# Kernel tuning notes

Hardware: AMD Instinct MI355X
Metric: run time of the kernel (lower is better)

The kernel has to match this reference:

```python
import jax, jax.numpy as jnp
import numpy as np

N_NODES = 50000
N_EDGES = 800000
EPS = 1e-16

def _gat_layer(x, row, col, W, a_src, a_dst, b, heads, concat):
    N = x.shape[0]
    C = a_src.shape[1]
    h = (x @ W).reshape(N, heads, C)                       # [N,H,C]
    al_src = jnp.sum(h * a_src, axis=-1)                    # [N,H]
    al_dst = jnp.sum(h * a_dst, axis=-1)                    # [N,H]
    e = jax.nn.leaky_relu(al_src[row] + al_dst[col], 0.2)   # [E,H]
    # segment softmax over destination node (col)
    m = jax.ops.segment_max(e, col, num_segments=N)
    e = jnp.exp(e - m[col])
    s = jax.ops.segment_sum(e, col, num_segments=N)
    alpha = e / (s[col] + EPS)                              # [E,H]
    msg = h[row] * alpha[:, :, None]                        # [E,H,C]
    out = jax.ops.segment_sum(msg, col, num_segments=N)     # [N,H,C]
    out = out.reshape(N, heads * C) if concat else out.mean(axis=1)
    return out + b

def setup_inputs() -> dict:
    key = jax.random.key(0)
    ks = jax.random.split(key, 16)
    d_in, hid, d_out, d_edge, H = 64, 64, 32, 16, 4
    inp = {
        "x": jax.random.normal(ks[0], (N_NODES, d_in), jnp.float32),
        "edge_index": jax.random.randint(ks[1], (2, N_EDGES), 0, N_NODES, jnp.int32),
        "edge_attr": jax.random.normal(ks[2], (N_EDGES, d_edge), jnp.float32),
        "W1": jax.random.normal(ks[3], (d_in, H * hid), jnp.float32) * 0.1,
        "a1_src": jax.random.normal(ks[4], (H, hid), jnp.float32) * 0.1,
        "a1_dst": jax.random.normal(ks[5], (H, hid), jnp.float32) * 0.1,
        "b1": jax.random.normal(ks[6], (H * hid,), jnp.float32) * 0.1,
        "W2": jax.random.normal(ks[7], (H * hid, hid), jnp.float32) * 0.05,
        "a2_src": jax.random.normal(ks[8], (1, hid), jnp.float32) * 0.1,
        "a2_dst": jax.random.normal(ks[9], (1, hid), jnp.float32) * 0.1,
        "b2": jax.random.normal(ks[10], (hid,), jnp.float32) * 0.1,
        "Wn": jax.random.normal(ks[11], (hid, d_out), jnp.float32) * 0.1,
        "bn": jax.random.normal(ks[12], (d_out,), jnp.float32) * 0.1,
        "We": jax.random.normal(ks[13], (2 * hid + d_edge, 1), jnp.float32) * 0.1,
        "be": jax.random.normal(ks[14], (1,), jnp.float32) * 0.1,
    }
    return inp

def reference(x, edge_index, edge_attr, W1, a1_src, a1_dst, b1, W2, a2_src, a2_dst, b2, Wn, bn, We, be):
    N = x.shape[0]
    row0, col0 = edge_index[0], edge_index[1]
    # PyG GATConv default: add self loops for message passing
    loops = jnp.arange(N, dtype=edge_index.dtype)
    row = jnp.concatenate([row0, loops])
    col = jnp.concatenate([col0, loops])
    h = jax.nn.elu(_gat_layer(x, row, col, W1, a1_src, a1_dst, b1, heads=4, concat=True))
    h = jax.nn.elu(_gat_layer(h, row, col, W2, a2_src, a2_dst, b2, heads=1, concat=False))
    node_out = h @ Wn + bn                                   # [N, out]
    edge_feat = jnp.concatenate([h[row0], h[col0], edge_attr], axis=1)  # [E, 2*hid+d_edge]
    edge_out = edge_feat @ We + be                           # [E, 1]
    return (node_out, edge_out)
```

## Files before the change

kernel.cpp:

```cpp
#include <hip/hip_runtime.h>
#include <hip/hip_bf16.h>

#define N_NODES 50000
#define N_EDGES 800000
#define N_TOT   850000
#define MAXD    128

#define NBUCK 196
#define BCAP  8192

typedef __hip_bfloat16 bf16;
typedef __attribute__((ext_vector_type(8))) short bf16x8;
typedef __attribute__((ext_vector_type(4))) float f32x4;

__device__ __forceinline__ unsigned short f2bu(float v){
  union { bf16 b; unsigned short u; } cv; cv.b = __float2bfloat16(v); return cv.u;
}
__device__ __forceinline__ float bflo(unsigned int d){ return __uint_as_float(d << 16); }
__device__ __forceinline__ float bfhi(unsigned int d){ return __uint_as_float(d & 0xffff0000u); }

__global__ __launch_bounds__(256) void wfrag_kernel(const float* __restrict__ W1, const float* __restrict__ W2,
    const float* __restrict__ a1s, const float* __restrict__ a1d,
    unsigned short* __restrict__ wf1, unsigned short* __restrict__ wf2,
    float* __restrict__ ws1, float* __restrict__ wd1, int* __restrict__ bcur){
  int b = blockIdx.x, tid = threadIdx.x;
  if (b < 128) {
    int i = b*256 + tid;
    if (i < 16384) {
      int k = i >> 8, n = i & 255;
      int kk = k >> 5, qq = (k >> 3) & 3, j = k & 7, nt = n >> 4, cc = n & 15;
      wf1[(((kk*16 + nt)*4 + qq)*16 + cc)*8 + j] = f2bu(W1[i]);
    } else {
      int i2 = i - 16384;
      int k = i2 >> 6, n = i2 & 63;
      int kk = k >> 5, qq = (k >> 3) & 3, j = k & 7, ch = n >> 4, cc = n & 15;
      wf2[(((kk*4 + ch)*4 + qq)*16 + cc)*8 + j] = f2bu(W2[i2]);
    }
  } else if (b == 128) {
    int k = tid >> 2, h = tid & 3;
    const float* wrow = W1 + k*256 + h*64;
    const float* as = a1s + h*64;
    const float* ad = a1d + h*64;
    float ss = 0.f, sd = 0.f;
    #pragma unroll 8
    for (int c = 0; c < 64; ++c) {
      float wv = wrow[c];
      ss = fmaf(wv, as[c], ss);
      sd = fmaf(wv, ad[c], sd);
    }
    ws1[k*4 + h] = ss;
    wd1[k*4 + h] = sd;
  } else {
    if (tid < NBUCK) bcur[tid] = 0;
  }
}

__global__ __launch_bounds__(256) void binscatter_kernel(const int* __restrict__ ei,
    int* __restrict__ bcur, unsigned int* __restrict__ pairbuf){
  __shared__ int hist[NBUCK];
  __shared__ int gbase[NBUCK];
  int tid = threadIdx.x;
  if (tid < NBUCK) hist[tid] = 0;
  __syncthreads();
  int base = blockIdx.x * 4096;
  #pragma unroll 4
  for (int i = 0; i < 16; ++i) {
    int k = base + i*256 + tid;
    if (k < N_TOT) {
      int c = (k < N_EDGES) ? ei[N_EDGES + k] : (k - N_EDGES);
      atomicAdd(&hist[c >> 8], 1);
    }
  }
  __syncthreads();
  if (tid < NBUCK) {
    int h = hist[tid];
    gbase[tid] = h ? (tid*BCAP + atomicAdd(&bcur[tid], h)) : 0;
    hist[tid] = 0;
  }
  __syncthreads();
  #pragma unroll 4
  for (int i = 0; i < 16; ++i) {
    int k = base + i*256 + tid;
    if (k < N_TOT) {
      int r, c;
      if (k < N_EDGES) { r = ei[k]; c = ei[N_EDGES + k]; } else { r = c = k - N_EDGES; }
      int b = c >> 8;
      int lpos = atomicAdd(&hist[b], 1);
      pairbuf[gbase[b] + lpos] = (unsigned)r | ((unsigned)(c & 255) << 16);
    }
  }
}

__global__ __launch_bounds__(256) void lscatter2_kernel(const unsigned int* __restrict__ pairbuf,
    const int* __restrict__ bcur, int* __restrict__ offs, int* __restrict__ srcs){
  __shared__ int sbase[256];
  __shared__ int lhist[256];
  __shared__ int lcur[256];
  int b = blockIdx.x, tid = threadIdx.x;
  int sz = 0;
  if (tid < NBUCK) {
    sz = bcur[tid];
    if (sz < 0) sz = 0; if (sz > BCAP) sz = BCAP;
  }
  sbase[tid] = sz;
  lhist[tid] = 0;
  __syncthreads();
  for (int off = 1; off < 256; off <<= 1) {
    int t = (tid >= off) ? sbase[tid - off] : 0;
    __syncthreads();
    sbase[tid] += t;
    __syncthreads();
  }
  int bbase_b = (b == 0) ? 0 : sbase[b - 1];
  int size = sbase[b] - bbase_b;
  int base = b * BCAP;
  for (int j = tid; j < size; j += 256)
    atomicAdd(&lhist[pairbuf[base + j] >> 16], 1);
  __syncthreads();
  int v = lhist[tid];
  lcur[tid] = v;
  __syncthreads();
  for (int off = 1; off < 256; off <<= 1) {
    int t = (tid >= off) ? lcur[tid - off] : 0;
    __syncthreads();
    lcur[tid] += t;
    __syncthreads();
  }
  int excl = lcur[tid] - v;
  int gpos = bbase_b + excl;
  int node = b*256 + tid;
  if (node < N_NODES) offs[node] = gpos;
  if (b == 0 && tid == 0) offs[N_NODES] = N_TOT;
  __syncthreads();
  lcur[tid] = gpos;
  __syncthreads();
  for (int j = tid; j < size; j += 256) {
    unsigned pv = pairbuf[base + j];
    int pos = atomicAdd(&lcur[pv >> 16], 1);
    srcs[pos] = (int)(pv & 0xFFFFu);
  }
}

__global__ __launch_bounds__(256) void xprep_kernel(const float* __restrict__ x,
    const float* __restrict__ ws1, const float* __restrict__ wd1,
    unsigned short* __restrict__ xb, float* __restrict__ al1s, float* __restrict__ al1d){
  __shared__ float sws[64][4], swd[64][4];
  int tid = threadIdx.x;
  sws[tid >> 2][tid & 3] = ws1[tid];
  swd[tid >> 2][tid & 3] = wd1[tid];
  __syncthreads();
  int lane = tid & 63, wave = tid >> 6;
  int g = lane & 15, sub = lane >> 4;
  int n = blockIdx.x*16 + wave*4 + sub;
  float4 xv = *(const float4*)(x + (size_t)n*64 + g*4);
  uint2 dd;
  dd.x = (unsigned)f2bu(xv.x) | ((unsigned)f2bu(xv.y) << 16);
  dd.y = (unsigned)f2bu(xv.z) | ((unsigned)f2bu(xv.w) << 16);
  ((uint2*)xb)[(size_t)n*16 + g] = dd;
  int c0 = g*4;
  float ps0 = 0.f, ps1 = 0.f, ps2 = 0.f, ps3 = 0.f;
  float pd0 = 0.f, pd1 = 0.f, pd2 = 0.f, pd3 = 0.f;
  float xc[4] = {xv.x, xv.y, xv.z, xv.w};
  #pragma unroll
  for (int i = 0; i < 4; ++i) {
    int c = c0 + i;
    ps0 = fmaf(xc[i], sws[c][0], ps0); ps1 = fmaf(xc[i], sws[c][1], ps1);
    ps2 = fmaf(xc[i], sws[c][2], ps2); ps3 = fmaf(xc[i], sws[c][3], ps3);
    pd0 = fmaf(xc[i], swd[c][0], pd0); pd1 = fmaf(xc[i], swd[c][1], pd1);
    pd2 = fmaf(xc[i], swd[c][2], pd2); pd3 = fmaf(xc[i], swd[c][3], pd3);
  }
  #pragma unroll
  for (int off = 1; off < 16; off <<= 1) {
    ps0 += __shfl_xor(ps0, off, 64); ps1 += __shfl_xor(ps1, off, 64);
    ps2 += __shfl_xor(ps2, off, 64); ps3 += __shfl_xor(ps3, off, 64);
    pd0 += __shfl_xor(pd0, off, 64); pd1 += __shfl_xor(pd1, off, 64);
    pd2 += __shfl_xor(pd2, off, 64); pd3 += __shfl_xor(pd3, off, 64);
  }
  if (g < 4)      al1s[(size_t)n*4 + g]       = (g==0)?ps0:(g==1)?ps1:(g==2)?ps2:ps3;
  else if (g < 8) al1d[(size_t)n*4 + (g-4)]   = (g==4)?pd0:(g==5)?pd1:(g==6)?pd2:pd3;
}

__global__ __launch_bounds__(256, 8) void attn1x_kernel(const unsigned short* __restrict__ xb,
    const float* __restrict__ al1s, const float* __restrict__ al1d,
    const int* __restrict__ offs, const int* __restrict__ srcs,
    bf16* __restrict__ ag){
  __shared__ __align__(16) float ebuf[4][MAXD+4][4];
  __shared__ int sbuf[4][MAXD+4];

  int wave = threadIdx.x >> 6, lane = threadIdx.x & 63;
  int n = blockIdx.x*4 + wave;
  int start = offs[n], end = offs[n+1];
  int deg = end - start;
  int lim = deg < MAXD ? deg : MAXD;
  float4 aldv = *(const float4*)(al1d + (size_t)n*4);
  float ald0 = aldv.x, ald1 = aldv.y, ald2 = aldv.z, ald3 = aldv.w;

  float s0 = 0.f, s1 = 0.f, s2 = 0.f, s3 = 0.f;
  {
    int idx = lane;
    for (int j = start + lane; j < end; j += 64, idx += 64) {
      int r = srcs[j];
      float4 als = *(const float4*)(al1s + (size_t)r*4);
      float e0 = als.x + ald0; e0 = e0 >= 0.f ? e0 : 0.2f*e0; float p0 = __expf(e0); s0 += p0;
      float e1 = als.y + ald1; e1 = e1 >= 0.f ? e1 : 0.2f*e1; float p1 = __expf(e1); s1 += p1;
      float e2 = als.z + ald2; e2 = e2 >= 0.f ? e2 : 0.2f*e2; float p2 = __expf(e2); s2 += p2;
      float e3 = als.w + ald3; e3 = e3 >= 0.f ? e3 : 0.2f*e3; float p3 = __expf(e3); s3 += p3;
      if (idx < MAXD) {
        sbuf[wave][idx] = r;
        *(float4*)&ebuf[wave][idx][0] = make_float4(p0, p1, p2, p3);
      }
    }
  }
  if (lane < 4) {
    int ip = lim + lane;
    sbuf[wave][ip] = 0;
    *(float4*)&ebuf[wave][ip][0] = make_float4(0.f, 0.f, 0.f, 0.f);
  }
  #pragma unroll
  for (int off = 32; off; off >>= 1) {
    s0 += __shfl_xor(s0, off, 64);
    s1 += __shfl_xor(s1, off, 64);
    s2 += __shfl_xor(s2, off, 64);
    s3 += __shfl_xor(s3, off, 64);
  }
  float inv0 = 1.f/(s0 + 1e-16f), inv1 = 1.f/(s1 + 1e-16f);
  float inv2 = 1.f/(s2 + 1e-16f), inv3 = 1.f/(s3 + 1e-16f);

  int cl = lane & 15, es = lane >> 4;
  float acc[4][4];
  #pragma unroll
  for (int h = 0; h < 4; ++h)
    #pragma unroll
    for (int i = 0; i < 4; ++i) acc[h][i] = 0.f;
  {
    const uint2* base2 = (const uint2*)xb;
    #pragma unroll 2
    for (int jj = 0; jj < lim; jj += 4) {
      int idx = jj + es;
      int r = sbuf[wave][idx];
      float4 pv = *(const float4*)&ebuf[wave][idx][0];
      uint2 d = base2[(size_t)r*16 + cl];
      float c0 = bflo(d.x), c1 = bfhi(d.x), c2 = bflo(d.y), c3 = bfhi(d.y);
      acc[0][0] = fmaf(pv.x, c0, acc[0][0]); acc[0][1] = fmaf(pv.x, c1, acc[0][1]);
      acc[0][2] = fmaf(pv.x, c2, acc[0][2]); acc[0][3] = fmaf(pv.x, c3, acc[0][3]);
      acc[1][0] = fmaf(pv.y, c0, acc[1][0]); acc[1][1] = fmaf(pv.y, c1, acc[1][1]);
      acc[1][2] = fmaf(pv.y, c2, acc[1][2]); acc[1][3] = fmaf(pv.y, c3, acc[1][3]);
      acc[2][0] = fmaf(pv.z, c0, acc[2][0]); acc[2][1] = fmaf(pv.z, c1, acc[2][1]);
      acc[2][2] = fmaf(pv.z, c2, acc[2][2]); acc[2][3] = fmaf(pv.z, c3, acc[2][3]);
      acc[3][0] = fmaf(pv.w, c0, acc[3][0]); acc[3][1] = fmaf(pv.w, c1, acc[3][1]);
      acc[3][2] = fmaf(pv.w, c2, acc[3][2]); acc[3][3] = fmaf(pv.w, c3, acc[3][3]);
    }
  }
  if (deg > MAXD) {
    const uint2* base2 = (const uint2*)xb;
    for (int jj = MAXD; jj < deg; jj += 4) {
      int idx = jj + es;
      bool ok = idx < deg;
      int j = ok ? (start + idx) : start;
      int r = srcs[j];
      float4 als = *(const float4*)(al1s + (size_t)r*4);
      float e0 = als.x + ald0; e0 = e0 >= 0.f ? e0 : 0.2f*e0; float p0 = __expf(e0);
      float e1 = als.y + ald1; e1 = e1 >= 0.f ? e1 : 0.2f*e1; float p1 = __expf(e1);
      float e2 = als.z + ald2; e2 = e2 >= 0.f ? e2 : 0.2f*e2; float p2 = __expf(e2);
      float e3 = als.w + ald3; e3 = e3 >= 0.f ? e3 : 0.2f*e3; float p3 = __expf(e3);
      float m = ok ? 1.f : 0.f;
      uint2 d = base2[(size_t)r*16 + cl];
      float c0 = bflo(d.x)*m, c1 = bfhi(d.x)*m, c2 = bflo(d.y)*m, c3 = bfhi(d.y)*m;
      acc[0][0] = fmaf(p0, c0, acc[0][0]); acc[0][1] = fmaf(p0, c1, acc[0][1]);
      acc[0][2] = fmaf(p0, c2, acc[0][2]); acc[0][3] = fmaf(p0, c3, acc[0][3]);
      acc[1][0] = fmaf(p1, c0, acc[1][0]); acc[1][1] = fmaf(p1, c1, acc[1][1]);
      acc[1][2] = fmaf(p1, c2, acc[1][2]); acc[1][3] = fmaf(p1, c3, acc[1][3]);
      acc[2][0] = fmaf(p2, c0, acc[2][0]); acc[2][1] = fmaf(p2, c1, acc[2][1]);
      acc[2][2] = fmaf(p2, c2, acc[2][2]); acc[2][3] = fmaf(p2, c3, acc[2][3]);
      acc[3][0] = fmaf(p3, c0, acc[3][0]); acc[3][1] = fmaf(p3, c1, acc[3][1]);
      acc[3][2] = fmaf(p3, c2, acc[3][2]); acc[3][3] = fmaf(p3, c3, acc[3][3]);
    }
  }
  #pragma unroll
  for (int h = 0; h < 4; ++h)
    #pragma unroll
    for (int i = 0; i < 4; ++i) {
      acc[h][i] += __shfl_xor(acc[h][i], 16, 64);
      acc[h][i] += __shfl_xor(acc[h][i], 32, 64);
    }
  {
    float invh = (es==0)?inv0:(es==1)?inv1:(es==2)?inv2:inv3;
    float o0 = ((es==0)?acc[0][0]:(es==1)?acc[1][0]:(es==2)?acc[2][0]:acc[3][0]) * invh;
    float o1 = ((es==0)?acc[0][1]:(es==1)?acc[1][1]:(es==2)?acc[2][1]:acc[3][1]) * invh;
    float o2 = ((es==0)?acc[0][2]:(es==1)?acc[1][2]:(es==2)?acc[2][2]:acc[3][2]) * invh;
    float o3 = ((es==0)?acc[0][3]:(es==1)?acc[1][3]:(es==2)?acc[2][3]:acc[3][3]) * invh;
    uint2 dd;
    dd.x = (unsigned)f2bu(o0) | ((unsigned)f2bu(o1) << 16);
    dd.y = (unsigned)f2bu(o2) | ((unsigned)f2bu(o3) << 16);
    ((uint2*)ag)[(size_t)n*64 + lane] = dd;
  }
}

__global__ __launch_bounds__(256) void gemm1b_kernel(const unsigned short* __restrict__ ag,
    const unsigned short* __restrict__ wf1, const float* __restrict__ b1, bf16* __restrict__ h1){
  __shared__ __align__(16) unsigned short ctile[32*264];
  int tid = threadIdx.x, wave = tid >> 6, lane = tid & 63;
  int q = lane >> 4, c = lane & 15;
  int n0 = blockIdx.x * 64;

  union { uint4 u; bf16x8 v; } bfr[2][4];
  #pragma unroll
  for (int kk = 0; kk < 2; ++kk)
    #pragma unroll
    for (int nti = 0; nti < 4; ++nti)
      bfr[kk][nti].u = *(const uint4*)(wf1 + (size_t)((((kk*16 + wave*4 + nti)*4 + q)*16 + c)*8));

  float b1v[4];
  #pragma unroll
  for (int nti = 0; nti < 4; ++nti) b1v[nti] = b1[(wave*4 + nti)*16 + c];

  #pragma unroll
  for (int half = 0; half < 2; ++half) {
    #pragma unroll
    for (int sti = 0; sti < 2; ++sti) {
      int st = half*2 + sti;
      int row = n0 + st*16 + c;
      if (row >= N_NODES) row = N_NODES - 1;
      bf16x8 afr[2];
      #pragma unroll
      for (int kk = 0; kk < 2; ++kk) {
        union { uint4 u; bf16x8 v; } a;
        a.u = *(const uint4*)(ag + (size_t)row*256 + wave*64 + kk*32 + q*8);
        afr[kk] = a.v;
      }
      #pragma unroll
      for (int nti = 0; nti < 4; ++nti) {
        f32x4 acc = {0.f, 0.f, 0.f, 0.f};
        #pragma unroll
        for (int kk = 0; kk < 2; ++kk)
          acc = __builtin_amdgcn_mfma_f32_16x16x32_bf16(afr[kk], bfr[kk][nti].v, acc, 0, 0, 0);
        int lrow = sti*16 + q*4, nt = wave*4 + nti;
        #pragma unroll
        for (int r = 0; r < 4; ++r) {
          float o = acc[r] + b1v[nti];
          o = o > 0.f ? o : expm1f(o);
          ctile[(lrow + r)*264 + nt*16 + c] = f2bu(o);
        }
      }
    }
    __syncthreads();
    #pragma unroll 1
    for (int i = 0; i < 8; ++i) {
      int lr = wave*8 + i;
      int node = n0 + half*32 + lr;
      if (node < N_NODES) {
        uint2 dd = *(const uint2*)&ctile[lr*264 + lane*4];
        ((uint2*)h1)[(size_t)node*64 + lane] = dd;
      }
    }
    __syncthreads();
  }
}

__global__ __launch_bounds__(256) void gemm2_kernel(const bf16* __restrict__ h1, const unsigned short* __restrict__ wf2,
    const float* __restrict__ a2s, const float* __restrict__ a2d,
    bf16* __restrict__ h2pre, float* __restrict__ al2s, float* __restrict__ al2d){
  __shared__ __align__(16) float ctile[64][65];
  int tid = threadIdx.x, wave = tid >> 6, lane = tid & 63;
  int q = lane >> 4, c = lane & 15;
  int n0 = blockIdx.x * 64;

  union { uint4 u; bf16x8 v; } bfr[8];
  #pragma unroll
  for (int kk = 0; kk < 8; ++kk)
    bfr[kk].u = *(const uint4*)(wf2 + (size_t)((((kk*4 + wave)*4 + q)*16 + c)*8));

  const unsigned short* h1u = (const unsigned short*)h1;
  #pragma unroll 1
  for (int st = 0; st < 4; ++st) {
    if (n0 + st*16 >= N_NODES) break;
    f32x4 acc = {0.f, 0.f, 0.f, 0.f};
    size_t arow = (size_t)(n0 + st*16 + c)*256 + q*8;
    #pragma unroll
    for (int kk = 0; kk < 8; ++kk) {
      union { uint4 u; bf16x8 v; } a;
      a.u = *(const uint4*)(h1u + arow + kk*32);
      acc = __builtin_amdgcn_mfma_f32_16x16x32_bf16(a.v, bfr[kk].v, acc, 0, 0, 0);
    }
    #pragma unroll
    for (int r = 0; r < 4; ++r)
      ctile[st*16 + q*4 + r][wave*16 + c] = acc[r];
  }
  __syncthreads();

  float as = a2s[lane], ad = a2d[lane];
  #pragma unroll 1
  for (int i = 0; i < 16; ++i) {
    int node = n0 + wave*16 + i;
    if (node >= N_NODES) break;
    float val = ctile[wave*16 + i][lane];
    ((unsigned short*)h2pre)[(size_t)node*64 + lane] = f2bu(val);
    float ps = val*as, pd = val*ad;
    #pragma unroll
    for (int off = 32; off; off >>= 1) { ps += __shfl_xor(ps, off, 64); pd += __shfl_xor(pd, off, 64); }
    if (lane == 0) { al2s[node] = ps; al2d[node] = pd; }
  }
}

__global__ __launch_bounds__(512, 8) void attn2_kernel(const bf16* __restrict__ h2pre,
    const float* __restrict__ al2s, const float* __restrict__ al2d,
    const int* __restrict__ offs, const int* __restrict__ srcs,
    const float* __restrict__ b2, float* __restrict__ h2f){
  __shared__ float ebuf[8][MAXD+8];
  __shared__ int   sbuf[8][MAXD+8];
  int wave = threadIdx.x >> 6, lane = threadIdx.x & 63;
  int n = blockIdx.x*8 + wave;
  int start = offs[n], end = offs[n+1];
  int deg = end - start;
  int lim = deg < MAXD ? deg : MAXD;
  float ald = al2d[n];

  float sm = 0.f;
  {
    int idx = lane;
    for (int j = start + lane; j < end; j += 64, idx += 64) {
      int r = srcs[j];
      float t = al2s[r] + ald; t = t >= 0.f ? t : 0.2f*t;
      float p = __expf(t); sm += p;
      if (idx < MAXD) { sbuf[wave][idx] = r; ebuf[wave][idx] = p; }
    }
  }
  if (lane < 8) { int ip = lim + lane; sbuf[wave][ip] = 0; ebuf[wave][ip] = 0.f; }
  #pragma unroll
  for (int off = 32; off; off >>= 1) sm += __shfl_xor(sm, off, 64);
  float inv = 1.f/(sm + 1e-16f);

  int cl = lane & 7, es = lane >> 3;
  float acc0 = 0.f, acc1 = 0.f, acc2 = 0.f, acc3 = 0.f;
  float acc4 = 0.f, acc5 = 0.f, acc6 = 0.f, acc7 = 0.f;
  {
    const uint4* base4 = (const uint4*)h2pre;
    #pragma unroll 2
    for (int jj = 0; jj < lim; jj += 8) {
      int idx = jj + es;
      int r = sbuf[wave][idx];
      float p = ebuf[wave][idx];
      uint4 d = base4[(size_t)r*8 + cl];
      acc0 = fmaf(p, bflo(d.x), acc0);
      acc1 = fmaf(p, bfhi(d.x), acc1);
      acc2 = fmaf(p, bflo(d.y), acc2);
      acc3 = fmaf(p, bfhi(d.y), acc3);
      acc4 = fmaf(p, bflo(d.z), acc4);
      acc5 = fmaf(p, bfhi(d.z), acc5);
      acc6 = fmaf(p, bflo(d.w), acc6);
      acc7 = fmaf(p, bfhi(d.w), acc7);
    }
  }
  if (deg > MAXD) {
    const uint4* base4 = (const uint4*)h2pre;
    for (int jj = MAXD; jj < deg; jj += 8) {
      int idx = jj + es;
      bool ok = idx < deg;
      int j = ok ? (start + idx) : start;
      int r = srcs[j];
      float t = al2s[r] + ald; t = t >= 0.f ? t : 0.2f*t;
      float p = ok ? __expf(t) : 0.f;
      uint4 d = base4[(size_t)r*8 + cl];
      acc0 = fmaf(p, bflo(d.x), acc0);
      acc1 = fmaf(p, bfhi(d.x), acc1);
      acc2 = fmaf(p, bflo(d.y), acc2);
      acc3 = fmaf(p, bfhi(d.y), acc3);
      acc4 = fmaf(p, bflo(d.z), acc4);
      acc5 = fmaf(p, bfhi(d.z), acc5);
      acc6 = fmaf(p, bflo(d.w), acc6);
      acc7 = fmaf(p, bfhi(d.w), acc7);
    }
  }
  #pragma unroll
  for (int off = 8; off < 64; off <<= 1) {
    acc0 += __shfl_xor(acc0, off, 64);
    acc1 += __shfl_xor(acc1, off, 64);
    acc2 += __shfl_xor(acc2, off, 64);
    acc3 += __shfl_xor(acc3, off, 64);
    acc4 += __shfl_xor(acc4, off, 64);
    acc5 += __shfl_xor(acc5, off, 64);
    acc6 += __shfl_xor(acc6, off, 64);
    acc7 += __shfl_xor(acc7, off, 64);
  }

  if (es == 0) {
    float4 b2a = *(const float4*)(b2 + cl*8);
    float4 b2b = *(const float4*)(b2 + cl*8 + 4);
    float o0 = acc0*inv + b2a.x; o0 = o0 > 0.f ? o0 : expm1f(o0);
    float o1 = acc1*inv + b2a.y; o1 = o1 > 0.f ? o1 : expm1f(o1);
    float o2 = acc2*inv + b2a.z; o2 = o2 > 0.f ? o2 : expm1f(o2);
    float o3 = acc3*inv + b2a.w; o3 = o3 > 0.f ? o3 : expm1f(o3);
    float o4 = acc4*inv + b2b.x; o4 = o4 > 0.f ? o4 : expm1f(o4);
    float o5 = acc5*inv + b2b.y; o5 = o5 > 0.f ? o5 : expm1f(o5);
    float o6 = acc6*inv + b2b.z; o6 = o6 > 0.f ? o6 : expm1f(o6);
    float o7 = acc7*inv + b2b.w; o7 = o7 > 0.f ? o7 : expm1f(o7);
    *(float4*)(h2f + (size_t)n*64 + cl*8)     = make_float4(o0, o1, o2, o3);
    *(float4*)(h2f + (size_t)n*64 + cl*8 + 4) = make_float4(o4, o5, o6, o7);
  }
}

__global__ __launch_bounds__(256) void head_kernel(const float* __restrict__ h2f,
    const float* __restrict__ Wn, const float* __restrict__ bn, const float* __restrict__ We,
    float* __restrict__ u, float* __restrict__ v, float* __restrict__ node_out){
  __shared__ __align__(16) float sh[8][64];
  int tid = threadIdx.x;
  int nb = blockIdx.x*8;
  {
    float2 t = *(const float2*)(h2f + (size_t)nb*64 + tid*2);
    *(float2*)&sh[tid >> 5][(tid & 31)*2] = t;
  }
  __syncthreads();
  int wave = tid >> 6, lane = tid & 63;
  int sub = lane >> 5, j = lane & 31;
  int local = wave*2 + sub;
  int n = nb + local;
  const float* h = sh[local];
  float a = 0.f;
  #pragma unroll 16
  for (int k = 0; k < 64; ++k)
    a = fmaf(h[k], Wn[k*32 + j], a);
  node_out[(size_t)n*32 + j] = a + bn[j];
  float pu = h[j]*We[j] + h[j+32]*We[j+32];
  float pv = h[j]*We[64+j] + h[j+32]*We[96+j];
  #pragma unroll
  for (int off = 1; off < 32; off <<= 1) {
    pu += __shfl_xor(pu, off, 64);
    pv += __shfl_xor(pv, off, 64);
  }
  if (j == 0) { u[n] = pu; v[n] = pv; }
}

__global__ __launch_bounds__(256) void edge_kernel(const int* __restrict__ ei, const float* __restrict__ ea,
    const float* __restrict__ u, const float* __restrict__ v,
    const float* __restrict__ We, const float* __restrict__ be, float* __restrict__ out){
  int k = blockIdx.x*256 + threadIdx.x;
  int r = ei[k], c = ei[N_EDGES + k];
  float val = u[r] + v[c] + be[0];
  const float4* wp = (const float4*)(We + 128);
  const float4* p  = (const float4*)(ea + (size_t)k*16);
  #pragma unroll
  for (int jj = 0; jj < 4; jj++) {
    float4 q = p[jj], wq = wp[jj];
    val = fmaf(q.x, wq.x, val);
    val = fmaf(q.y, wq.y, val);
    val = fmaf(q.z, wq.z, val);
    val = fmaf(q.w, wq.w, val);
  }
  out[k] = val;
}

extern "C" void kernel_launch(void* const* d_in, const int* in_sizes, int n_in,
                              void* d_out, int out_size, void* d_ws, size_t ws_size,
                              hipStream_t stream) {
  const float* x   = (const float*)d_in[0];
  const int*   ei  = (const int*)d_in[1];
  const float* ea  = (const float*)d_in[2];
  const float* W1  = (const float*)d_in[3];
  const float* a1s = (const float*)d_in[4];
  const float* a1d = (const float*)d_in[5];
  const float* b1  = (const float*)d_in[6];
  const float* W2  = (const float*)d_in[7];
  const float* a2s = (const float*)d_in[8];
  const float* a2d = (const float*)d_in[9];
  const float* b2  = (const float*)d_in[10];
  const float* Wn  = (const float*)d_in[11];
  const float* bn  = (const float*)d_in[12];
  const float* We  = (const float*)d_in[13];
  const float* be  = (const float*)d_in[14];
  float* out = (float*)d_out;

  char* w = (char*)d_ws;
  int*   offs   = (int*)(w);
  unsigned short* wf1 = (unsigned short*)(w + 200016);
  float* ws1    = (float*)(w + 232784);
  float* wd1    = (float*)(w + 233808);
  unsigned short* wf2 = (unsigned short*)(w + 234832);
  int*   bcur   = (int*)(w + 400016);
  int*   srcs   = (int*)(w + 600016);
  float* al1s   = (float*)(w + 4000016);
  float* al1d   = (float*)(w + 4800016);
  float* al2s   = (float*)(w + 5600016);
  float* al2d   = (float*)(w + 5800016);
  float* uu     = (float*)(w + 6000016);
  float* vv     = (float*)(w + 6200016);
  bf16*  h2pre  = (bf16*)(w + 6400016);
  bf16*  ag     = (bf16*)(w + 12800016);
  bf16*  h1     = (bf16*)(w + 38400224);
  unsigned short* xb  = (unsigned short*)h2pre;
  unsigned int* pairbuf = (unsigned int*)h1;
  float* h2f = (float*)ag;

  wfrag_kernel     <<<130, 256, 0, stream>>>(W1, W2, a1s, a1d, wf1, wf2, ws1, wd1, bcur);
  binscatter_kernel<<<(N_TOT + 4095)/4096, 256, 0, stream>>>(ei, bcur, pairbuf);
  lscatter2_kernel <<<NBUCK, 256, 0, stream>>>(pairbuf, bcur, offs, srcs);
  xprep_kernel     <<<N_NODES/16, 256, 0, stream>>>(x, ws1, wd1, xb, al1s, al1d);
  attn1x_kernel    <<<N_NODES/4, 256, 0, stream>>>(xb, al1s, al1d, offs, srcs, ag);
  gemm1b_kernel    <<<(N_NODES + 63)/64, 256, 0, stream>>>((const unsigned short*)ag, wf1, b1, h1);
  gemm2_kernel     <<<(N_NODES + 63)/64, 256, 0, stream>>>(h1, wf2, a2s, a2d, h2pre, al2s, al2d);
  attn2_kernel     <<<N_NODES/8, 512, 0, stream>>>(h2pre, al2s, al2d, offs, srcs, b2, h2f);
  head_kernel      <<<N_NODES/8, 256, 0, stream>>>(h2f, Wn, bn, We, uu, vv, out);
  edge_kernel      <<<N_EDGES/256, 256, 0, stream>>>(ei, ea, uu, vv, We, be, out + (size_t)N_NODES*32);
}
```

Measured before the change: 312.9 us.

## Fuse layer-1 output GEMM with layer-2 GEMM through shared memory

Merges gemm1b and gemm2 into one kernel. The ELU-activated h1 tile (64 rows x 256 bf16) stays in LDS and feeds the layer-2 MFMA directly, so h1 is never written to or read back from global memory and one launch is removed. In exchange, LDS use per block rises to about 50KB, which may lower occupancy. The dedicated h1 buffer is dropped and pairbuf takes its place.

```diff
diff --git a/kernel.cpp b/kernel.cpp
--- a/kernel.cpp
+++ b/kernel.cpp
@@ -296,29 +296,30 @@
   }
 }
 
-__global__ __launch_bounds__(256) void gemm1b_kernel(const unsigned short* __restrict__ ag,
-    const unsigned short* __restrict__ wf1, const float* __restrict__ b1, bf16* __restrict__ h1){
-  __shared__ __align__(16) unsigned short ctile[32*264];
+__global__ __launch_bounds__(256) void gemm12_kernel(const unsigned short* __restrict__ ag,
+    const unsigned short* __restrict__ wf1, const unsigned short* __restrict__ wf2,
+    const float* __restrict__ b1, const float* __restrict__ a2s, const float* __restrict__ a2d,
+    bf16* __restrict__ h2pre, float* __restrict__ al2s, float* __restrict__ al2d){
+  __shared__ __align__(16) unsigned short ctile[64*264];
+  __shared__ __align__(16) float ctile2[64][65];
   int tid = threadIdx.x, wave = tid >> 6, lane = tid & 63;
   int q = lane >> 4, c = lane & 15;
   int n0 = blockIdx.x * 64;
 
-  union { uint4 u; bf16x8 v; } bfr[2][4];
-  #pragma unroll
-  for (int kk = 0; kk < 2; ++kk)
+  {
+    union { uint4 u; bf16x8 v; } bfr[2][4];
     #pragma unroll
-    for (int nti = 0; nti < 4; ++nti)
-      bfr[kk][nti].u = *(const uint4*)(wf1 + (size_t)((((kk*16 + wave*4 + nti)*4 + q)*16 + c)*8));
-
-  float b1v[4];
-  #pragma unroll
-  for (int nti = 0; nti < 4; ++nti) b1v[nti] = b1[(wave*4 + nti)*16 + c];
-
-  #pragma unroll
-  for (int half = 0; half < 2; ++half) {
+    for (int kk = 0; kk < 2; ++kk)
+      #pragma unroll
+      for (int nti = 0; nti < 4; ++nti)
+        bfr[kk][nti].u = *(const uint4*)(wf1 + (size_t)((((kk*16 + wave*4 + nti)*4 + q)*16 + c)*8));
+
+    float b1v[4];
     #pragma unroll
-    for (int sti = 0; sti < 2; ++sti) {
-      int st = half*2 + sti;
+    for (int nti = 0; nti < 4; ++nti) b1v[nti] = b1[(wave*4 + nti)*16 + c];
+
+    #pragma unroll 1
+    for (int st = 0; st < 4; ++st) {
       int row = n0 + st*16 + c;
       if (row >= N_NODES) row = N_NODES - 1;
       bf16x8 afr[2];
@@ -334,7 +335,7 @@
         #pragma unroll
         for (int kk = 0; kk < 2; ++kk)
           acc = __builtin_amdgcn_mfma_f32_16x16x32_bf16(afr[kk], bfr[kk][nti].v, acc, 0, 0, 0);
-        int lrow = sti*16 + q*4, nt = wave*4 + nti;
+        int lrow = st*16 + q*4, nt = wave*4 + nti;
         #pragma unroll
         for (int r = 0; r < 4; ++r) {
           float o = acc[r] + b1v[nti];
@@ -343,48 +344,30 @@
         }
       }
     }
-    __syncthreads();
+  }
+  __syncthreads();
+
+  {
+    union { uint4 u; bf16x8 v; } bfr[8];
+    #pragma unroll
+    for (int kk = 0; kk < 8; ++kk)
+      bfr[kk].u = *(const uint4*)(wf2 + (size_t)((((kk*4 + wave)*4 + q)*16 + c)*8));
+
     #pragma unroll 1
-    for (int i = 0; i < 8; ++i) {
-      int lr = wave*8 + i;
-      int node = n0 + half*32 + lr;
-      if (node < N_NODES) {
-        uint2 dd = *(const uint2*)&ctile[lr*264 + lane*4];
-        ((uint2*)h1)[(size_t)node*64 + lane] = dd;
+    for (int st = 0; st < 4; ++st) {
+      if (n0 + st*16 >= N_NODES) break;
+      f32x4 acc = {0.f, 0.f, 0.f, 0.f};
+      int arow = (st*16 + c)*264 + q*8;
+      #pragma unroll
+      for (int kk = 0; kk < 8; ++kk) {
+        union { uint4 u; bf16x8 v; } a;
+        a.u = *(const uint4*)&ctile[arow + kk*32];
+        acc = __builtin_amdgcn_mfma_f32_16x16x32_bf16(a.v, bfr[kk].v, acc, 0, 0, 0);
       }
-    }
-    __syncthreads();
-  }
-}
-
-__global__ __launch_bounds__(256) void gemm2_kernel(const bf16* __restrict__ h1, const unsigned short* __restrict__ wf2,
-    const float* __restrict__ a2s, const float* __restrict__ a2d,
-    bf16* __restrict__ h2pre, float* __restrict__ al2s, float* __restrict__ al2d){
-  __shared__ __align__(16) float ctile[64][65];
-  int tid = threadIdx.x, wave = tid >> 6, lane = tid & 63;
-  int q = lane >> 4, c = lane & 15;
-  int n0 = blockIdx.x * 64;
-
-  union { uint4 u; bf16x8 v; } bfr[8];
-  #pragma unroll
-  for (int kk = 0; kk < 8; ++kk)
-    bfr[kk].u = *(const uint4*)(wf2 + (size_t)((((kk*4 + wave)*4 + q)*16 + c)*8));
-
-  const unsigned short* h1u = (const unsigned short*)h1;
-  #pragma unroll 1
-  for (int st = 0; st < 4; ++st) {
-    if (n0 + st*16 >= N_NODES) break;
-    f32x4 acc = {0.f, 0.f, 0.f, 0.f};
-    size_t arow = (size_t)(n0 + st*16 + c)*256 + q*8;
-    #pragma unroll
-    for (int kk = 0; kk < 8; ++kk) {
-      union { uint4 u; bf16x8 v; } a;
-      a.u = *(const uint4*)(h1u + arow + kk*32);
-      acc = __builtin_amdgcn_mfma_f32_16x16x32_bf16(a.v, bfr[kk].v, acc, 0, 0, 0);
-    }
-    #pragma unroll
-    for (int r = 0; r < 4; ++r)
-      ctile[st*16 + q*4 + r][wave*16 + c] = acc[r];
+      #pragma unroll
+      for (int r = 0; r < 4; ++r)
+        ctile2[st*16 + q*4 + r][wave*16 + c] = acc[r];
+    }
   }
   __syncthreads();
 
@@ -393,7 +376,7 @@
   for (int i = 0; i < 16; ++i) {
     int node = n0 + wave*16 + i;
     if (node >= N_NODES) break;
-    float val = ctile[wave*16 + i][lane];
+    float val = ctile2[wave*16 + i][lane];
     ((unsigned short*)h2pre)[(size_t)node*64 + lane] = f2bu(val);
     float ps = val*as, pd = val*ad;
     #pragma unroll
@@ -585,9 +568,8 @@
   float* vv     = (float*)(w + 6200016);
   bf16*  h2pre  = (bf16*)(w + 6400016);
   bf16*  ag     = (bf16*)(w + 12800016);
-  bf16*  h1     = (bf16*)(w + 38400224);
+  unsigned int* pairbuf = (unsigned int*)(w + 38400224);
   unsigned short* xb  = (unsigned short*)h2pre;
-  unsigned int* pairbuf = (unsigned int*)h1;
   float* h2f = (float*)ag;
 
   wfrag_kernel     <<<130, 256, 0, stream>>>(W1, W2, a1s, a1d, wf1, wf2, ws1, wd1, bcur);
@@ -595,8 +577,8 @@
   lscatter2_kernel <<<NBUCK, 256, 0, stream>>>(pairbuf, bcur, offs, srcs);
   xprep_kernel     <<<N_NODES/16, 256, 0, stream>>>(x, ws1, wd1, xb, al1s, al1d);
   attn1x_kernel    <<<N_NODES/4, 256, 0, stream>>>(xb, al1s, al1d, offs, srcs, ag);
-  gemm1b_kernel    <<<(N_NODES + 63)/64, 256, 0, stream>>>((const unsigned short*)ag, wf1, b1, h1);
-  gemm2_kernel     <<<(N_NODES + 63)/64, 256, 0, stream>>>(h1, wf2, a2s, a2d, h2pre, al2s, al2d);
+  gemm12_kernel    <<<(N_NODES + 63)/64, 256, 0, stream>>>((const unsigned short*)ag, wf1, wf2, b1,
+                                                           a2s, a2d, h2pre, al2s, al2d);
   attn2_kernel     <<<N_NODES/8, 512, 0, stream>>>(h2pre, al2s, al2d, offs, srcs, b2, h2f);
   head_kernel      <<<N_NODES/8, 256, 0, stream>>>(h2f, Wn, bn, We, uu, vv, out);
   edge_kernel      <<<N_EDGES/256, 256, 0, stream>>>(ei, ea, uu, vv, We, be, out + (size_t)N_NODES*32);
```

Result: faster. 301.7 us (-3.6%).
